# Kernel tuning notes

Measured on AMD Instinct MI355X. Metric: run time of the kernel, lower is better.

## Reference

```python
import jax, jax.numpy as jnp
import numpy as np

T, E = 16384, 1024   # frames, feature dim (WavLM-Large)
M, K = 8, 512        # number of kmeans models, clusters per model


def setup_inputs() -> dict:
    key = jax.random.key(0)
    k1, k2, k3 = jax.random.split(key, 3)
    emb = jax.random.normal(k1, (1, T, E), dtype=jnp.float32)
    centroids = jax.random.normal(k2, (M, K, E), dtype=jnp.float32)
    # per-frame random kmeans model choice (stride=1): replaces random.randint in the loop
    model_idx = jax.random.randint(k3, (T,), 0, M, dtype=jnp.int32)
    return {"emb": emb, "centroids": centroids, "model_idx": model_idx}


def reference(emb, centroids, model_idx):
    # emb: [1,T,E], centroids: [M,K,E], model_idx: [T] in [0,M)
    x = emb[0]  # [T,E]
    # squared euclidean distance from every frame to every centroid of every model
    # (argmin over squared dist == argmin over cdist)
    x_sq = jnp.sum(x * x, axis=-1)                      # [T]
    c_sq = jnp.sum(centroids * centroids, axis=-1)      # [M,K]
    dots = jnp.einsum('te,mke->tmk', x, centroids)      # [T,M,K]
    d_all = x_sq[:, None, None] - 2.0 * dots + c_sq[None, :, :]  # [T,M,K]
    # select the randomly chosen model's distances per frame
    d = jnp.take_along_axis(d_all, model_idx[:, None, None].astype(jnp.int32), axis=1)[:, 0, :]  # [T,K]
    codes = jnp.argmin(d, axis=-1)                      # [T]
    # embedding lookup: the quantizer's emb maps cluster id -> centroid vector
    out = centroids[model_idx, codes]                   # [T,E]
    return out[None]  # [1,T,E]
```

## Files before the change

### kernel.cpp

```cpp
#include <hip/hip_runtime.h>


#define T_FRAMES 16384
#define E_DIM    1024
#define M_MODELS 8
#define K_CLUST  512

#define FPB 32
#define NCH 8

typedef __bf16 bf16x8 __attribute__((ext_vector_type(8)));
typedef float  floatx16 __attribute__((ext_vector_type(16)));

__device__ __forceinline__ bf16x8 cvt8(const float4 a, const float4 b) {
  bf16x8 h;
  h[0] = (__bf16)a.x; h[1] = (__bf16)a.y; h[2] = (__bf16)a.z; h[3] = (__bf16)a.w;
  h[4] = (__bf16)b.x; h[5] = (__bf16)b.y; h[6] = (__bf16)b.z; h[7] = (__bf16)b.w;
  return h;
}

__global__ __launch_bounds__(256) void k_csq(const float* __restrict__ cent,
                                             double* __restrict__ csq64) {
  const int row = blockIdx.x * 4 + (threadIdx.x >> 6);
  const int lane = threadIdx.x & 63;
  const float* p = cent + (size_t)row * E_DIM;
  double s = 0.0;
#pragma unroll
  for (int i = 0; i < 16; ++i) {
    const float v = p[lane + i * 64];
    s += (double)v * (double)v;
  }
#pragma unroll
  for (int m = 32; m >= 1; m >>= 1) s += __shfl_xor(s, m, 64);
  if (lane == 0) csq64[row] = s;
}

__global__ __launch_bounds__(256) void k_cvt(const float* __restrict__ cent,
                                             float* __restrict__ out) {
  const int b = blockIdx.x;
  const int m = b >> 6;
  const int cg = (b >> 2) & 15;
  const int q = b & 3;
  const int tid = threadIdx.x;
  const int ci = tid & 31;
  const int gk0 = q * 32 + (tid >> 5) * 4;
  const int B32 = (m * 16 + cg) * 32;
  const float* src = cent + ((size_t)(m * K_CLUST + cg * 32 + ci)) * E_DIM;
#pragma unroll
  for (int j = 0; j < 4; ++j) {
    const int gk = gk0 + j;
    const float4 a = *(const float4*)(src + gk * 8);
    const float4 bb = *(const float4*)(src + gk * 8 + 4);
    const size_t foff = (size_t)(B32 + (gk >> 2)) * 1024 + 512 +
                        ((gk & 3) * 32 + ci) * 4;
    *(bf16x8*)(out + foff) = cvt8(a, bb);
  }
}

__global__ __launch_bounds__(256) void k_hist(const int* __restrict__ midx,
                                              int* __restrict__ hist) {
  __shared__ int h[M_MODELS * 33];
  const int tid = threadIdx.x;
  for (int i = tid; i < M_MODELS * 33; i += 256) h[i] = 0;
  __syncthreads();
  const int m = midx[blockIdx.x * 256 + tid];
  atomicAdd(&h[m * 33 + (tid & 31)], 1);
  __syncthreads();
  if (tid < M_MODELS) {
    int s = 0;
    for (int j = 0; j < 32; ++j) s += h[tid * 33 + j];
    hist[blockIdx.x * M_MODELS + tid] = s;
  }
}

__global__ __launch_bounds__(256) void k_scatter(const int* __restrict__ midx,
                                                 const int* __restrict__ hist,
                                                 int* __restrict__ order,
                                                 int* __restrict__ offs) {
  __shared__ int h2[64 * M_MODELS];
  __shared__ int cur[M_MODELS];
  const int tid = threadIdx.x;
  h2[tid] = hist[tid];
  h2[tid + 256] = hist[tid + 256];
  __syncthreads();
  if (tid < M_MODELS) {
    int tot_before = 0;
    for (int mp = 0; mp < tid; ++mp)
      for (int b = 0; b < 64; ++b) tot_before += h2[b * M_MODELS + mp];
    int prior = 0;
    for (int b = 0; b < (int)blockIdx.x; ++b) prior += h2[b * M_MODELS + tid];
    cur[tid] = tot_before + prior;
  }
  if (blockIdx.x == 0 && tid <= M_MODELS) {
    int o = 0;
    for (int mp = 0; mp < tid; ++mp)
      for (int b = 0; b < 64; ++b) o += h2[b * M_MODELS + mp];
    offs[tid] = o;
  }
  __syncthreads();
  const int f = blockIdx.x * 256 + tid;
  const int pos = atomicAdd(&cur[midx[f]], 1);
  order[pos] = f;
}

__global__ __launch_bounds__(512, 4) void k_dist(const float* __restrict__ emb,
                                                 const float* __restrict__ cent,
                                                 const double* __restrict__ csq64,
                                                 const int* __restrict__ order,
                                                 const int* __restrict__ offs,
                                                 float* __restrict__ out) {
  const int m = blockIdx.x;
  const int o0 = offs[m];
  const int cnt = offs[m + 1] - o0;
  const int start = blockIdx.y * FPB;
  if (start >= cnt) return;
  const int nvalid = min(FPB, cnt - start);

  __shared__ __align__(16) __bf16 A_l[2 * 16 * FPB * 8];
  __shared__ int rows_l[FPB];
  __shared__ float wmin_s[8][FPB];
  __shared__ int wcol_s[8][FPB];
  __shared__ float gmin_s[FPB];
  __shared__ int cnt_s[FPB];
  __shared__ int cand_s[FPB][32];

  const int tid = threadIdx.x;
  const int l = tid & 63;
  const int w = tid >> 6;
  const int ln = l & 31;
  const int lh = l >> 5;

  if (tid < FPB) rows_l[tid] = order[o0 + start + min(tid, nvalid - 1)];
  __syncthreads();

  const int s_row = tid & 31;
  const int s_g = tid >> 5;
  const float4* emb4 = (const float4*)emb;
  const size_t arow4 = (size_t)rows_l[s_row] * (E_DIM / 4);

  float4 pa[2];
  pa[0] = emb4[arow4 + s_g * 2 + 0];
  pa[1] = emb4[arow4 + s_g * 2 + 1];
  *(bf16x8*)(A_l + ((s_g)*FPB + s_row) * 8) = cvt8(pa[0], pa[1]);

  const char* bbase[2];
#pragma unroll
  for (int ct = 0; ct < 2; ++ct) {
    const int cg = w * 2 + ct;
    bbase[ct] = (const char*)out + (size_t)(m * 16 + cg) * 131072 + 2048 + l * 16;
  }
#define LOADB(ct, kb) (*(const bf16x8*)(bbase[ct] + (((kb) >> 1) << 12) + (((kb) & 1) << 10)))

  bf16x8 bR[4][2];
#pragma unroll
  for (int d = 0; d < 4; ++d)
#pragma unroll
    for (int ct = 0; ct < 2; ++ct) bR[d][ct] = LOADB(ct, d);

  floatx16 acc[2] = {};

  for (int c = 0; c < NCH; ++c) {
    __syncthreads();
    const int buf = (c & 1) * 16;
    if (c + 1 < NCH) {
      pa[0] = emb4[arow4 + (c + 1) * 32 + s_g * 2 + 0];
      pa[1] = emb4[arow4 + (c + 1) * 32 + s_g * 2 + 1];
    }
#pragma unroll
    for (int jj = 0; jj < 8; ++jj) {
      const int kb = c * 8 + jj;
      const int p = kb & 3;
      const bf16x8 a0 = *(const bf16x8*)(A_l + ((buf + jj * 2 + lh) * FPB + ln) * 8);
      acc[0] = __builtin_amdgcn_mfma_f32_32x32x16_bf16(a0, bR[p][0], acc[0], 0, 0, 0);
      acc[1] = __builtin_amdgcn_mfma_f32_32x32x16_bf16(a0, bR[p][1], acc[1], 0, 0, 0);
      if (kb + 4 < 64) {
        bR[p][0] = LOADB(0, kb + 4);
        bR[p][1] = LOADB(1, kb + 4);
      }
    }
    if (c + 1 < NCH) {
      const int nbuf = ((c + 1) & 1) * 16;
      *(bf16x8*)(A_l + ((nbuf + s_g) * FPB + s_row) * 8) = cvt8(pa[0], pa[1]);
    }
  }
#undef LOADB

  float cs[2];
#pragma unroll
  for (int ct = 0; ct < 2; ++ct)
    cs[ct] = (float)csq64[m * K_CLUST + w * 64 + ct * 32 + ln];

#pragma unroll
  for (int r = 0; r < 16; ++r) {
    const int fr = (r & 3) + 8 * (r >> 2) + 4 * lh;
    float bm = cs[0] - 2.0f * acc[0][r];
    int bc = w * 64 + ln;
    {
      const float s = cs[1] - 2.0f * acc[1][r];
      if (s < bm) { bm = s; bc = w * 64 + 32 + ln; }
    }
#pragma unroll
    for (int sh = 1; sh <= 16; sh <<= 1) {
      const float om = __shfl_xor(bm, sh, 64);
      const int oc = __shfl_xor(bc, sh, 64);
      if (om < bm || (om == bm && oc < bc)) { bm = om; bc = oc; }
    }
    if (ln == 0) { wmin_s[w][fr] = bm; wcol_s[w][fr] = bc; }
  }
  __syncthreads();

  if (tid < FPB) {
    float g = wmin_s[0][tid];
    int gc = wcol_s[0][tid];
#pragma unroll
    for (int w2 = 1; w2 < 8; ++w2) {
      const float v = wmin_s[w2][tid];
      const int vc = wcol_s[w2][tid];
      if (v < g || (v == g && vc < gc)) { g = v; gc = vc; }
    }
    gmin_s[tid] = g;
    cnt_s[tid] = 0;
  }
  __syncthreads();

#pragma unroll
  for (int r = 0; r < 16; ++r) {
    const int fr = (r & 3) + 8 * (r >> 2) + 4 * lh;
    const float thr = gmin_s[fr] + 3.0f;
#pragma unroll
    for (int ct = 0; ct < 2; ++ct) {
      const float s = cs[ct] - 2.0f * acc[ct][r];
      if (s < thr) {
        const int ix = atomicAdd(&cnt_s[fr], 1);
        if (ix < 32) cand_s[fr][ix] = w * 64 + ct * 32 + ln;
      }
    }
  }
  __syncthreads();

  for (int i = 0; i < 4; ++i) {
    const int f = w * 4 + i;
    const int t = rows_l[f];
    const int n = min(cnt_s[f], 32);
    int code;
    if (n == 1) {
      code = cand_s[f][0];
    } else {
      float4 xv[4];
#pragma unroll
      for (int q = 0; q < 4; ++q) xv[q] = emb4[(size_t)t * (E_DIM / 4) + q * 64 + l];
      double bd = 1e300;
      int bi = 1 << 30;
      for (int j = 0; j < n; ++j) {
        const int cc = cand_s[f][j];
        const float4* crow4 = (const float4*)(cent + ((size_t)(m * K_CLUST + cc)) * E_DIM);
        double s = 0.0;
#pragma unroll
        for (int q = 0; q < 4; ++q) {
          const float4 cv = crow4[q * 64 + l];
          s += (double)xv[q].x * cv.x + (double)xv[q].y * cv.y +
               (double)xv[q].z * cv.z + (double)xv[q].w * cv.w;
        }
#pragma unroll
        for (int sh = 32; sh >= 1; sh >>= 1) s += __shfl_xor(s, sh, 64);
        const double d = csq64[m * K_CLUST + cc] - 2.0 * s;
        if (d < bd || (d == bd && cc < bi)) { bd = d; bi = cc; }
      }
      code = bi;
    }
    if (l == 0) *(int*)(out + (size_t)t * E_DIM) = code;
  }
}

__global__ __launch_bounds__(256) void k_gather(const float* __restrict__ cent,
                                                const int* __restrict__ midx,
                                                float* __restrict__ out) {
  const int t = blockIdx.x * 4 + (threadIdx.x >> 6);
  const int l = threadIdx.x & 63;
  float* drow = out + (size_t)t * E_DIM;
  const int code = *(const int*)drow;
  const int m = midx[t];
  const float4* src = (const float4*)(cent + ((size_t)(m * K_CLUST + code)) * E_DIM);
  float4* dst = (float4*)drow;
#pragma unroll
  for (int q = 0; q < 4; ++q) dst[q * 64 + l] = src[q * 64 + l];
}

extern "C" void kernel_launch(void* const* d_in, const int* in_sizes, int n_in,
                              void* d_out, int out_size, void* d_ws, size_t ws_size,
                              hipStream_t stream) {
  const float* emb = (const float*)d_in[0];
  const float* cent = (const float*)d_in[1];
  const int* midx = (const int*)d_in[2];
  float* out = (float*)d_out;

  char* ws = (char*)d_ws;
  double* csq64 = (double*)(ws + 0);
  int* hist = (int*)(ws + 32768);
  int* offs = (int*)(ws + 34816);
  int* order = (int*)(ws + 34880);

  hipLaunchKernelGGL(k_cvt, dim3(512), dim3(256), 0, stream, cent, out);
  hipLaunchKernelGGL(k_csq, dim3(1024), dim3(256), 0, stream, cent, csq64);
  hipLaunchKernelGGL(k_hist, dim3(64), dim3(256), 0, stream, midx, hist);
  hipLaunchKernelGGL(k_scatter, dim3(64), dim3(256), 0, stream, midx, hist, order, offs);
  hipLaunchKernelGGL(k_dist, dim3(M_MODELS, 80), dim3(512), 0, stream,
                     emb, cent, csq64, order, offs, out);
  hipLaunchKernelGGL(k_gather, dim3(T_FRAMES / 4), dim3(256), 0, stream,
                     cent, midx, out);
}
```

Before: 205.6 us.

## Fuse centroid-norm into conversion kernel and stage whole emb tile up front

```diff
diff --git a/kernel.cpp b/kernel.cpp
--- a/kernel.cpp
+++ b/kernel.cpp
@@ -7,7 +7,6 @@
 #define K_CLUST  512
 
 #define FPB 32
-#define NCH 8
 
 typedef __bf16 bf16x8 __attribute__((ext_vector_type(8)));
 typedef float  floatx16 __attribute__((ext_vector_type(16)));
@@ -19,41 +18,40 @@
   return h;
 }
 
-__global__ __launch_bounds__(256) void k_csq(const float* __restrict__ cent,
+__global__ __launch_bounds__(256) void k_cvt(const float* __restrict__ cent,
+                                             float* __restrict__ out,
                                              double* __restrict__ csq64) {
-  const int row = blockIdx.x * 4 + (threadIdx.x >> 6);
-  const int lane = threadIdx.x & 63;
-  const float* p = cent + (size_t)row * E_DIM;
-  double s = 0.0;
-#pragma unroll
-  for (int i = 0; i < 16; ++i) {
-    const float v = p[lane + i * 64];
-    s += (double)v * (double)v;
-  }
-#pragma unroll
-  for (int m = 32; m >= 1; m >>= 1) s += __shfl_xor(s, m, 64);
-  if (lane == 0) csq64[row] = s;
-}
-
-__global__ __launch_bounds__(256) void k_cvt(const float* __restrict__ cent,
-                                             float* __restrict__ out) {
   const int b = blockIdx.x;
   const int m = b >> 6;
   const int cg = (b >> 2) & 15;
   const int q = b & 3;
   const int tid = threadIdx.x;
   const int ci = tid & 31;
-  const int gk0 = q * 32 + (tid >> 5) * 4;
+  const int t8 = tid >> 5;
+  const int gk0 = q * 32 + t8 * 4;
   const int B32 = (m * 16 + cg) * 32;
   const float* src = cent + ((size_t)(m * K_CLUST + cg * 32 + ci)) * E_DIM;
+  double ss = 0.0;
 #pragma unroll
   for (int j = 0; j < 4; ++j) {
     const int gk = gk0 + j;
     const float4 a = *(const float4*)(src + gk * 8);
     const float4 bb = *(const float4*)(src + gk * 8 + 4);
+    ss += (double)a.x * a.x + (double)a.y * a.y + (double)a.z * a.z +
+          (double)a.w * a.w + (double)bb.x * bb.x + (double)bb.y * bb.y +
+          (double)bb.z * bb.z + (double)bb.w * bb.w;
     const size_t foff = (size_t)(B32 + (gk >> 2)) * 1024 + 512 +
                         ((gk & 3) * 32 + ci) * 4;
     *(bf16x8*)(out + foff) = cvt8(a, bb);
+  }
+  __shared__ double csq_l[32][8];
+  csq_l[ci][t8] = ss;
+  __syncthreads();
+  if (tid < 32) {
+    double s = 0.0;
+#pragma unroll
+    for (int t = 0; t < 8; ++t) s += csq_l[tid][t];
+    atomicAdd(&csq64[m * K_CLUST + cg * 32 + tid], s);
   }
 }
 
@@ -116,7 +114,7 @@
   if (start >= cnt) return;
   const int nvalid = min(FPB, cnt - start);
 
-  __shared__ __align__(16) __bf16 A_l[2 * 16 * FPB * 8];
+  __shared__ __align__(16) __bf16 A_l[128 * FPB * 8];
   __shared__ int rows_l[FPB];
   __shared__ float wmin_s[8][FPB];
   __shared__ int wcol_s[8][FPB];
@@ -134,14 +132,17 @@
   __syncthreads();
 
   const int s_row = tid & 31;
-  const int s_g = tid >> 5;
+  const int s_gb = tid >> 5;
   const float4* emb4 = (const float4*)emb;
   const size_t arow4 = (size_t)rows_l[s_row] * (E_DIM / 4);
 
-  float4 pa[2];
-  pa[0] = emb4[arow4 + s_g * 2 + 0];
-  pa[1] = emb4[arow4 + s_g * 2 + 1];
-  *(bf16x8*)(A_l + ((s_g)*FPB + s_row) * 8) = cvt8(pa[0], pa[1]);
+  float4 pa[16];
+#pragma unroll
+  for (int j = 0; j < 16; ++j) pa[j] = emb4[arow4 + s_gb * 16 + j];
+#pragma unroll
+  for (int j = 0; j < 8; ++j)
+    *(bf16x8*)(A_l + ((s_gb * 8 + j) * FPB + s_row) * 8) =
+        cvt8(pa[2 * j], pa[2 * j + 1]);
 
   const char* bbase[2];
 #pragma unroll
@@ -157,30 +158,18 @@
 #pragma unroll
     for (int ct = 0; ct < 2; ++ct) bR[d][ct] = LOADB(ct, d);
 
+  __syncthreads();
+
   floatx16 acc[2] = {};
-
-  for (int c = 0; c < NCH; ++c) {
-    __syncthreads();
-    const int buf = (c & 1) * 16;
-    if (c + 1 < NCH) {
-      pa[0] = emb4[arow4 + (c + 1) * 32 + s_g * 2 + 0];
-      pa[1] = emb4[arow4 + (c + 1) * 32 + s_g * 2 + 1];
-    }
-#pragma unroll
-    for (int jj = 0; jj < 8; ++jj) {
-      const int kb = c * 8 + jj;
-      const int p = kb & 3;
-      const bf16x8 a0 = *(const bf16x8*)(A_l + ((buf + jj * 2 + lh) * FPB + ln) * 8);
-      acc[0] = __builtin_amdgcn_mfma_f32_32x32x16_bf16(a0, bR[p][0], acc[0], 0, 0, 0);
-      acc[1] = __builtin_amdgcn_mfma_f32_32x32x16_bf16(a0, bR[p][1], acc[1], 0, 0, 0);
-      if (kb + 4 < 64) {
-        bR[p][0] = LOADB(0, kb + 4);
-        bR[p][1] = LOADB(1, kb + 4);
-      }
-    }
-    if (c + 1 < NCH) {
-      const int nbuf = ((c + 1) & 1) * 16;
-      *(bf16x8*)(A_l + ((nbuf + s_g) * FPB + s_row) * 8) = cvt8(pa[0], pa[1]);
+#pragma unroll
+  for (int kb = 0; kb < 64; ++kb) {
+    const int p = kb & 3;
+    const bf16x8 a0 = *(const bf16x8*)(A_l + ((kb * 2 + lh) * FPB + ln) * 8);
+    acc[0] = __builtin_amdgcn_mfma_f32_32x32x16_bf16(a0, bR[p][0], acc[0], 0, 0, 0);
+    acc[1] = __builtin_amdgcn_mfma_f32_32x32x16_bf16(a0, bR[p][1], acc[1], 0, 0, 0);
+    if (kb + 4 < 64) {
+      bR[p][0] = LOADB(0, kb + 4);
+      bR[p][1] = LOADB(1, kb + 4);
     }
   }
 #undef LOADB
@@ -300,8 +289,8 @@
   int* offs = (int*)(ws + 34816);
   int* order = (int*)(ws + 34880);
 
-  hipLaunchKernelGGL(k_cvt, dim3(512), dim3(256), 0, stream, cent, out);
-  hipLaunchKernelGGL(k_csq, dim3(1024), dim3(256), 0, stream, cent, csq64);
+  hipMemsetAsync(csq64, 0, M_MODELS * K_CLUST * sizeof(double), stream);
+  hipLaunchKernelGGL(k_cvt, dim3(512), dim3(256), 0, stream, cent, out, csq64);
   hipLaunchKernelGGL(k_hist, dim3(64), dim3(256), 0, stream, midx, hist);
   hipLaunchKernelGGL(k_scatter, dim3(64), dim3(256), 0, stream, midx, hist, order, offs);
   hipLaunchKernelGGL(k_dist, dim3(M_MODELS, 80), dim3(512), 0, stream,
```

Result: slower. 219.3 us (+6.7%).

## Fuse centroid norm into convert kernel and fold gather into distance kernel

Applied to the files above, without the earlier changes.

```diff
diff --git a/kernel.cpp b/kernel.cpp
--- a/kernel.cpp
+++ b/kernel.cpp
@@ -19,48 +19,49 @@
   return h;
 }
 
-__global__ __launch_bounds__(256) void k_csq(const float* __restrict__ cent,
+__global__ __launch_bounds__(256) void k_cvt(const float* __restrict__ cent,
+                                             float* __restrict__ out,
                                              double* __restrict__ csq64) {
-  const int row = blockIdx.x * 4 + (threadIdx.x >> 6);
-  const int lane = threadIdx.x & 63;
-  const float* p = cent + (size_t)row * E_DIM;
-  double s = 0.0;
-#pragma unroll
-  for (int i = 0; i < 16; ++i) {
-    const float v = p[lane + i * 64];
-    s += (double)v * (double)v;
-  }
-#pragma unroll
-  for (int m = 32; m >= 1; m >>= 1) s += __shfl_xor(s, m, 64);
-  if (lane == 0) csq64[row] = s;
-}
-
-__global__ __launch_bounds__(256) void k_cvt(const float* __restrict__ cent,
-                                             float* __restrict__ out) {
   const int b = blockIdx.x;
   const int m = b >> 6;
   const int cg = (b >> 2) & 15;
   const int q = b & 3;
   const int tid = threadIdx.x;
   const int ci = tid & 31;
-  const int gk0 = q * 32 + (tid >> 5) * 4;
+  const int t8 = tid >> 5;
+  const int gk0 = q * 32 + t8 * 4;
   const int B32 = (m * 16 + cg) * 32;
   const float* src = cent + ((size_t)(m * K_CLUST + cg * 32 + ci)) * E_DIM;
+  double ss = 0.0;
 #pragma unroll
   for (int j = 0; j < 4; ++j) {
     const int gk = gk0 + j;
     const float4 a = *(const float4*)(src + gk * 8);
     const float4 bb = *(const float4*)(src + gk * 8 + 4);
+    ss += (double)a.x * a.x + (double)a.y * a.y + (double)a.z * a.z +
+          (double)a.w * a.w + (double)bb.x * bb.x + (double)bb.y * bb.y +
+          (double)bb.z * bb.z + (double)bb.w * bb.w;
     const size_t foff = (size_t)(B32 + (gk >> 2)) * 1024 + 512 +
                         ((gk & 3) * 32 + ci) * 4;
     *(bf16x8*)(out + foff) = cvt8(a, bb);
   }
+  __shared__ double csq_l[32][8];
+  csq_l[ci][t8] = ss;
+  __syncthreads();
+  if (tid < 32) {
+    double s = 0.0;
+#pragma unroll
+    for (int t = 0; t < 8; ++t) s += csq_l[tid][t];
+    atomicAdd(&csq64[m * K_CLUST + cg * 32 + tid], s);
+  }
 }
 
 __global__ __launch_bounds__(256) void k_hist(const int* __restrict__ midx,
-                                              int* __restrict__ hist) {
+                                              int* __restrict__ hist,
+                                              double* __restrict__ csq64) {
   __shared__ int h[M_MODELS * 33];
   const int tid = threadIdx.x;
+  if (tid < 64) csq64[blockIdx.x * 64 + tid] = 0.0;
   for (int i = tid; i < M_MODELS * 33; i += 256) h[i] = 0;
   __syncthreads();
   const int m = midx[blockIdx.x * 256 + tid];
@@ -268,7 +269,14 @@
       }
       code = bi;
     }
-    if (l == 0) *(int*)(out + (size_t)t * E_DIM) = code;
+    if (t >= 4096) {
+      const float4* crow = (const float4*)(cent + ((size_t)(m * K_CLUST + code)) * E_DIM);
+      float4* drow = (float4*)(out + (size_t)t * E_DIM);
+#pragma unroll
+      for (int q = 0; q < 4; ++q) drow[q * 64 + l] = crow[q * 64 + l];
+    } else if (l == 0) {
+      *(int*)(out + (size_t)t * E_DIM) = code;
+    }
   }
 }
 
@@ -300,12 +308,11 @@
   int* offs = (int*)(ws + 34816);
   int* order = (int*)(ws + 34880);
 
-  hipLaunchKernelGGL(k_cvt, dim3(512), dim3(256), 0, stream, cent, out);
-  hipLaunchKernelGGL(k_csq, dim3(1024), dim3(256), 0, stream, cent, csq64);
-  hipLaunchKernelGGL(k_hist, dim3(64), dim3(256), 0, stream, midx, hist);
+  hipLaunchKernelGGL(k_hist, dim3(64), dim3(256), 0, stream, midx, hist, csq64);
   hipLaunchKernelGGL(k_scatter, dim3(64), dim3(256), 0, stream, midx, hist, order, offs);
+  hipLaunchKernelGGL(k_cvt, dim3(512), dim3(256), 0, stream, cent, out, csq64);
   hipLaunchKernelGGL(k_dist, dim3(M_MODELS, 80), dim3(512), 0, stream,
                      emb, cent, csq64, order, offs, out);
-  hipLaunchKernelGGL(k_gather, dim3(T_FRAMES / 4), dim3(256), 0, stream,
+  hipLaunchKernelGGL(k_gather, dim3(4096 / 4), dim3(256), 0, stream,
                      cent, midx, out);
 }
```

Result: no change. 202.4 us (-1.6%).
